# Kernel tuning notes

Hardware: AMD Instinct MI355X
Metric: run time of the kernel (lower is better)

## Reference

```python
import jax, jax.numpy as jnp
import numpy as np

D_MODEL = 2048
NUM_HEADS = 16
NUM_KV_HEADS = 4
HEAD_DIM = D_MODEL // NUM_HEADS          # 128
GROUPS = NUM_HEADS // NUM_KV_HEADS       # 4
ROT_DIM = HEAD_DIM // 2                  # 64
QK_EPS = 1e-6
B, L = 2, 2048


def setup_inputs() -> dict:
    key = jax.random.key(0)
    kx, kq, kk, kv, ko = jax.random.split(key, 5)
    x = jax.random.normal(kx, (B, L, D_MODEL), dtype=jnp.float32)
    # realistic RoPE tables, broadcastable against [B, L, H, ROT_DIM]
    inv_freq = 1.0 / (10000.0 ** (np.arange(ROT_DIM, dtype=np.float32) / ROT_DIM))
    ang = np.arange(L, dtype=np.float32)[:, None] * inv_freq[None, :]   # [L, ROT_DIM]
    cos = jnp.asarray(np.cos(ang), dtype=jnp.float32)[None, :, None, :]
    sin = jnp.asarray(np.sin(ang), dtype=jnp.float32)[None, :, None, :]
    s = 1.0 / np.sqrt(D_MODEL)
    Wq = jax.random.normal(kq, (D_MODEL, D_MODEL), dtype=jnp.float32) * s
    Wk = jax.random.normal(kk, (D_MODEL, NUM_KV_HEADS * HEAD_DIM), dtype=jnp.float32) * s
    Wv = jax.random.normal(kv, (D_MODEL, NUM_KV_HEADS * HEAD_DIM), dtype=jnp.float32) * s
    Wo = jax.random.normal(ko, (D_MODEL, D_MODEL), dtype=jnp.float32) * s
    return {"x": x, "cos": cos, "sin": sin, "Wq": Wq, "Wk": Wk, "Wv": Wv, "Wo": Wo}


def _apply_rope(t, cos, sin):
    # t: [B, L, H, HEAD_DIM]; half-split rotation as in the original
    x1, x2 = t[..., :ROT_DIM], t[..., ROT_DIM:]
    return jnp.concatenate([x1 * cos - x2 * sin, x2 * cos + x1 * sin], axis=-1)


def _rms_norm(t):
    ms = jnp.mean(jnp.square(t), axis=-1, keepdims=True)
    return t * jax.lax.rsqrt(ms + QK_EPS)


def reference(x, cos, sin, Wq, Wk, Wv, Wo):
    b, l, _ = x.shape
    q = (x @ Wq).reshape(b, l, NUM_HEADS, HEAD_DIM)
    k = (x @ Wk).reshape(b, l, NUM_KV_HEADS, HEAD_DIM)
    v = (x @ Wv).reshape(b, l, NUM_KV_HEADS, HEAD_DIM)
    q = _apply_rope(q, cos, sin)
    k = _apply_rope(k, cos, sin)
    # qk_norm=True: RMS-normalize q and k over head_dim
    q = _rms_norm(q)
    k = _rms_norm(k)
    # GQA: repeat kv heads to match q heads (matches reshape/tile/reshape)
    k = jnp.repeat(k, GROUPS, axis=2)   # [b, l, NUM_HEADS, HEAD_DIM]
    v = jnp.repeat(v, GROUPS, axis=2)
    scores = jnp.einsum('blhd,bmhd->bhlm', q, k) / np.float32(np.sqrt(HEAD_DIM))
    causal = jnp.tril(jnp.ones((l, l), dtype=bool))[None, None, :, :]
    scores = jnp.where(causal, scores, jnp.float32(-1e9))
    attn = jax.nn.softmax(scores, axis=-1)            # [b, h, l(q), m(kv)]
    out = jnp.einsum('bhlm,bmhd->blhd', attn, v).reshape(b, l, D_MODEL)
    return out @ Wo
```

## Files before the change

kernel.cpp:

```cpp
#include <hip/hip_runtime.h>
#include <stdint.h>

#define D_MODEL 2048
#define L_SEQ   2048
#define BATCH   2
#define NH      16
#define NKV     4
#define HD      128
#define ROT     64
#define M_ROWS  (BATCH * L_SEQ)
#define N_QKV   (D_MODEL + 2 * NKV * HD)

typedef short bf16x8 __attribute__((ext_vector_type(8)));
typedef float f32x4  __attribute__((ext_vector_type(4)));
typedef float f32x16 __attribute__((ext_vector_type(16)));

__device__ __forceinline__ unsigned short f2b(float f) {
  union { float f; unsigned u; } v; v.f = f;
  unsigned r = v.u + 0x7FFFu + ((v.u >> 16) & 1u);
  return (unsigned short)(r >> 16);
}

__device__ __forceinline__ unsigned cvtpk_bf16(float a, float b) {
  unsigned r;
  asm("v_cvt_pk_bf16_f32 %0, %1, %2" : "=v"(r) : "v"(a), "v"(b));
  return r;
}

__global__ void cvt_bf16_kernel(const float* __restrict__ in,
                                unsigned short* __restrict__ out, int n4) {
  int i = blockIdx.x * blockDim.x + threadIdx.x;
  if (i < n4) {
    float4 v = ((const float4*)in)[i];
    ushort4 o;
    o.x = f2b(v.x); o.y = f2b(v.y); o.z = f2b(v.z); o.w = f2b(v.w);
    ((ushort4*)out)[i] = o;
  }
}

__global__ void build_wqkv_t(const float* __restrict__ Wq, const float* __restrict__ Wk,
                             const float* __restrict__ Wv, unsigned short* __restrict__ Wt) {
  __shared__ float tile[32][33];
  int k0 = blockIdx.x * 32;
  int n0 = blockIdx.y * 32;
  const float* W; int c0, ldw;
  if (n0 < D_MODEL)            { W = Wq; c0 = n0;                 ldw = D_MODEL; }
  else if (n0 < D_MODEL + 512) { W = Wk; c0 = n0 - D_MODEL;       ldw = 512; }
  else                         { W = Wv; c0 = n0 - D_MODEL - 512; ldw = 512; }
  int tx = threadIdx.x, ty = threadIdx.y;
#pragma unroll
  for (int i = 0; i < 32; i += 8)
    tile[ty + i][tx] = W[(size_t)(k0 + ty + i) * ldw + c0 + tx];
  __syncthreads();
#pragma unroll
  for (int i = 0; i < 32; i += 8)
    Wt[(size_t)(n0 + ty + i) * D_MODEL + k0 + tx] = f2b(tile[tx][ty + i]);
}

__global__ void build_wo_t(const float* __restrict__ Wo, unsigned short* __restrict__ Wt) {
  __shared__ float tile[32][33];
  int k0 = blockIdx.x * 32;
  int n0 = blockIdx.y * 32;
  int tx = threadIdx.x, ty = threadIdx.y;
#pragma unroll
  for (int i = 0; i < 32; i += 8)
    tile[ty + i][tx] = Wo[(size_t)(k0 + ty + i) * D_MODEL + n0 + tx];
  __syncthreads();
#pragma unroll
  for (int i = 0; i < 32; i += 8)
    Wt[(size_t)(n0 + ty + i) * D_MODEL + k0 + tx] = f2b(tile[tx][ty + i]);
}

#define BM 128
#define BN 128
#define BKg 64

__device__ __forceinline__ void async16(void* lds, const void* g) {
  __builtin_amdgcn_global_load_lds((const __attribute__((address_space(1))) void*)g,
                                   (__attribute__((address_space(3))) void*)lds, 16, 0, 0);
}

__global__ __launch_bounds__(256, 2)
void gemm_bt(const unsigned short* __restrict__ A, const unsigned short* __restrict__ Bt,
             float* __restrict__ C, int M, int N, int K) {
  __shared__ unsigned short As[BM * BKg];
  __shared__ unsigned short Bs[BN * BKg];
  int m0 = blockIdx.y * BM;
  int n0 = blockIdx.x * BN;
  int tid = threadIdx.x;
  int lane = tid & 63;
  int wave = __builtin_amdgcn_readfirstlane(tid >> 6);
  int wr = wave >> 1, wc = wave & 1;
  int lgrp = lane >> 4, lidx = lane & 15;

  f32x4 acc[4][4];
#pragma unroll
  for (int i = 0; i < 4; i++)
#pragma unroll
    for (int j = 0; j < 4; j++) { acc[i][j][0]=0.f; acc[i][j][1]=0.f; acc[i][j][2]=0.f; acc[i][j][3]=0.f; }

  for (int k0 = 0; k0 < K; k0 += BKg) {
#pragma unroll
    for (int iss = 0; iss < 4; iss++) {
      int idx = iss * 256 + tid;
      int row = idx >> 3, cch = idx & 7;
      int lbase = (iss * 256 + wave * 64) * 8;
      async16((void*)(As + lbase), A  + (size_t)(m0 + row) * K + k0 + cch * 8);
      async16((void*)(Bs + lbase), Bt + (size_t)(n0 + row) * K + k0 + cch * 8);
    }
    __syncthreads();
#pragma unroll
    for (int kk = 0; kk < BKg; kk += 32) {
      bf16x8 af[4], bfr[4];
#pragma unroll
      for (int i = 0; i < 4; i++) {
        af[i]  = *(const bf16x8*)(As + (wr * 64 + i * 16 + lidx) * BKg + kk + lgrp * 8);
        bfr[i] = *(const bf16x8*)(Bs + (wc * 64 + i * 16 + lidx) * BKg + kk + lgrp * 8);
      }
#pragma unroll
      for (int i = 0; i < 4; i++)
#pragma unroll
        for (int j = 0; j < 4; j++)
          acc[i][j] = __builtin_amdgcn_mfma_f32_16x16x32_bf16(af[i], bfr[j], acc[i][j], 0, 0, 0);
    }
    __syncthreads();
  }
#pragma unroll
  for (int i = 0; i < 4; i++) {
    int rowb = m0 + wr * 64 + i * 16 + lgrp * 4;
#pragma unroll
    for (int j = 0; j < 4; j++) {
      int col = n0 + wc * 64 + j * 16 + lidx;
#pragma unroll
      for (int r = 0; r < 4; r++)
        C[(size_t)(rowb + r) * N + col] = acc[i][j][r];
    }
  }
}

__global__ __launch_bounds__(256)
void rope_rms_kernel(const float* __restrict__ QKV, const float* __restrict__ cosp,
                     const float* __restrict__ sinp, unsigned short* __restrict__ Qb,
                     unsigned short* __restrict__ Kb) {
  int row = blockIdx.x;
  int b = row >> 11, l = row & 2047;
  int lane = threadIdx.x & 63;
  int wave = threadIdx.x >> 6;
  const float* src = QKV + (size_t)row * N_QKV;
  float c = cosp[l * ROT + lane];
  float s = sinp[l * ROT + lane];
  for (int hh = wave; hh < NH + NKV; hh += 4) {
    bool isq = hh < NH;
    int col0 = isq ? hh * HD : D_MODEL + (hh - NH) * HD;
    float x1 = src[col0 + lane];
    float x2 = src[col0 + 64 + lane];
    float o1 = x1 * c - x2 * s;
    float o2 = x2 * c + x1 * s;
    float ss = o1 * o1 + o2 * o2;
#pragma unroll
    for (int mk = 1; mk < 64; mk <<= 1) ss += __shfl_xor(ss, mk, 64);
    float rn = rsqrtf(ss * (1.f / 128.f) + 1e-6f);
    if (isq) rn *= 0.08838834764831845f;
    o1 *= rn; o2 *= rn;
    unsigned short* dst = isq ? (Qb + ((size_t)(b * NH + hh) * L_SEQ + l) * HD)
                              : (Kb + ((size_t)(b * NKV + (hh - NH)) * L_SEQ + l) * HD);
    dst[lane]      = f2b(o1);
    dst[lane + 64] = f2b(o2);
  }
}

__global__ void vt_build(const float* __restrict__ QKV, unsigned short* __restrict__ Vt) {
  __shared__ float tile[32][33];
  int z = blockIdx.z;
  int l0 = blockIdx.x * 32;
  int d0 = blockIdx.y * 32;
  int b = z >> 2, kh = z & 3;
  int tx = threadIdx.x, ty = threadIdx.y;
  int colbase = D_MODEL + NKV * HD + kh * HD + d0;
#pragma unroll
  for (int i = 0; i < 32; i += 8)
    tile[ty + i][tx] = QKV[(size_t)(b * L_SEQ + l0 + ty + i) * N_QKV + colbase + tx];
  __syncthreads();
#pragma unroll
  for (int i = 0; i < 32; i += 8)
    Vt[((size_t)z * HD + d0 + ty + i) * L_SEQ + l0 + tx] = f2b(tile[tx][ty + i]);
}

__global__ __launch_bounds__(64)
void attn32_kernel(const unsigned short* __restrict__ Qb, const unsigned short* __restrict__ Kb,
                   const unsigned short* __restrict__ Vt, unsigned short* __restrict__ AttO) {
  __shared__ float tr[32][33];
  int idx = blockIdx.x;
  int qb = 63 - (idx >> 5);
  int bh = idx & 31;
  int b = bh >> 4, h = bh & 15, kh = h >> 2;
  int q0 = qb * 32;
  int lane = threadIdx.x;
  int col = lane & 31;
  int hi  = lane >> 5;

  const unsigned short* Q = Qb + ((size_t)(b * NH + h) * L_SEQ + q0) * HD;
  const unsigned short* K = Kb + (size_t)(b * NKV + kh) * L_SEQ * HD;
  const unsigned short* V = Vt + (size_t)(b * NKV + kh) * HD * L_SEQ;

  bf16x8 qf[8];
#pragma unroll
  for (int c = 0; c < 8; c++)
    qf[c] = *(const bf16x8*)(Q + (size_t)col * HD + c * 16 + hi * 8);

  f32x16 o[4];
#pragma unroll
  for (int d0 = 0; d0 < 4; d0++)
#pragma unroll
    for (int r = 0; r < 16; r++) o[d0][r] = 0.f;

  float m = -1e30f, lsum = 0.f;

  for (int kv0 = 0; kv0 <= q0; kv0 += 32) {
    f32x16 s;
#pragma unroll
    for (int r = 0; r < 16; r++) s[r] = 0.f;
#pragma unroll
    for (int c = 0; c < 8; c++) {
      bf16x8 kf = *(const bf16x8*)(K + (size_t)(kv0 + col) * HD + c * 16 + hi * 8);
      s = __builtin_amdgcn_mfma_f32_32x32x16_bf16(kf, qf[c], s, 0, 0, 0);
    }
    if (kv0 == q0) {
#pragma unroll
      for (int r = 0; r < 16; r++) {
        int kvl = (r & 3) + 8 * (r >> 2) + 4 * hi;
        if (kvl > col) s[r] = -1e30f;
      }
    }
    float mx = s[0];
#pragma unroll
    for (int r = 1; r < 16; r++) mx = fmaxf(mx, s[r]);
    mx = fmaxf(mx, __shfl_xor(mx, 32, 64));
    if (!__all(mx <= m + 8.f)) {
      float mnew = fmaxf(m, mx);
      float sf = __expf(m - mnew);
      lsum *= sf;
#pragma unroll
      for (int d0 = 0; d0 < 4; d0++)
#pragma unroll
        for (int r = 0; r < 16; r++) o[d0][r] *= sf;
      m = mnew;
    }
    float p[16];
    float ps = 0.f;
#pragma unroll
    for (int r = 0; r < 16; r++) { p[r] = __expf(s[r] - m); ps += p[r]; }
    lsum += ps + __shfl_xor(ps, 32, 64);
#pragma unroll
    for (int w = 0; w < 2; w++) {
      unsigned c01 = cvtpk_bf16(p[w*8+0], p[w*8+1]);
      unsigned c23 = cvtpk_bf16(p[w*8+2], p[w*8+3]);
      unsigned c45 = cvtpk_bf16(p[w*8+4], p[w*8+5]);
      unsigned c67 = cvtpk_bf16(p[w*8+6], p[w*8+7]);
      unsigned x01 = (unsigned)__shfl_xor((int)c01, 32, 64);
      unsigned x23 = (unsigned)__shfl_xor((int)c23, 32, 64);
      unsigned x45 = (unsigned)__shfl_xor((int)c45, 32, 64);
      unsigned x67 = (unsigned)__shfl_xor((int)c67, 32, 64);
      union { unsigned u[4]; bf16x8 v; } pb;
      pb.u[0] = hi ? x45 : c01;
      pb.u[1] = hi ? x67 : c23;
      pb.u[2] = hi ? c45 : x01;
      pb.u[3] = hi ? c67 : x23;
#pragma unroll
      for (int d0 = 0; d0 < 4; d0++) {
        bf16x8 vf = *(const bf16x8*)(V + (size_t)(d0 * 32 + col) * L_SEQ + kv0 + w * 16 + hi * 8);
        o[d0] = __builtin_amdgcn_mfma_f32_32x32x16_bf16(vf, pb.v, o[d0], 0, 0, 0);
      }
    }
  }

  float inv = 1.f / lsum;
  unsigned short* orow = AttO + (size_t)(b * L_SEQ + q0 + col) * D_MODEL + h * HD;
#pragma unroll
  for (int d0 = 0; d0 < 4; d0++) {
#pragma unroll
    for (int r = 0; r < 16; r++)
      tr[(r & 3) + 8 * (r >> 2) + 4 * hi][col] = o[d0][r] * inv;
    __syncthreads();
    union { unsigned u[8]; } pk;
#pragma unroll
    for (int t = 0; t < 8; t++) {
      float a  = tr[hi * 16 + 2 * t][col];
      float bb = tr[hi * 16 + 2 * t + 1][col];
      pk.u[t] = ((unsigned)f2b(a)) | (((unsigned)f2b(bb)) << 16);
    }
    *(uint4*)(orow + d0 * 32 + hi * 16)     = *(uint4*)&pk.u[0];
    *(uint4*)(orow + d0 * 32 + hi * 16 + 8) = *(uint4*)&pk.u[4];
    __syncthreads();
  }
}

extern "C" void kernel_launch(void* const* d_in, const int* in_sizes, int n_in,
                              void* d_out, int out_size, void* d_ws, size_t ws_size,
                              hipStream_t stream) {
  const float* x    = (const float*)d_in[0];
  const float* cosp = (const float*)d_in[1];
  const float* sinp = (const float*)d_in[2];
  const float* Wq   = (const float*)d_in[3];
  const float* Wk   = (const float*)d_in[4];
  const float* Wv   = (const float*)d_in[5];
  const float* Wo   = (const float*)d_in[6];
  float* out = (float*)d_out;

  char* ws = (char*)d_ws;
  unsigned short* Xb   = (unsigned short*)ws; ws += (size_t)M_ROWS * D_MODEL * 2;
  unsigned short* Wt   = (unsigned short*)ws; ws += (size_t)N_QKV * D_MODEL * 2;
  unsigned short* Wot  = (unsigned short*)ws; ws += (size_t)D_MODEL * D_MODEL * 2;
  float*          QKV  = (float*)ws;          ws += (size_t)M_ROWS * N_QKV * 4;
  unsigned short* Qb   = (unsigned short*)ws; ws += (size_t)BATCH * NH * L_SEQ * HD * 2;
  unsigned short* Kb   = (unsigned short*)ws; ws += (size_t)BATCH * NKV * L_SEQ * HD * 2;
  unsigned short* Vt   = (unsigned short*)ws; ws += (size_t)BATCH * NKV * HD * L_SEQ * 2;
  unsigned short* AttO = (unsigned short*)ws; ws += (size_t)M_ROWS * D_MODEL * 2;

  cvt_bf16_kernel<<<(M_ROWS * D_MODEL / 4 + 255) / 256, 256, 0, stream>>>(x, Xb, M_ROWS * D_MODEL / 4);
  build_wqkv_t<<<dim3(64, 96), dim3(32, 8), 0, stream>>>(Wq, Wk, Wv, Wt);
  build_wo_t<<<dim3(64, 64), dim3(32, 8), 0, stream>>>(Wo, Wot);
  gemm_bt<<<dim3(N_QKV / BN, M_ROWS / BM), 256, 0, stream>>>(Xb, Wt, QKV, M_ROWS, N_QKV, D_MODEL);
  rope_rms_kernel<<<M_ROWS, 256, 0, stream>>>(QKV, cosp, sinp, Qb, Kb);
  vt_build<<<dim3(64, 4, 8), dim3(32, 8), 0, stream>>>(QKV, Vt);
  attn32_kernel<<<dim3(64 * 32), 64, 0, stream>>>(Qb, Kb, Vt, AttO);
  gemm_bt<<<dim3(D_MODEL / BN, M_ROWS / BM), 256, 0, stream>>>(AttO, Wot, out, M_ROWS, D_MODEL, D_MODEL);
}
```

Baseline: 395.5 us.

## Share K/V tiles across four waves via double-buffered async LDS staging

Replaces the one-wave, 32-query attention kernel with a 256-thread block covering 128 query rows. Each K/V tile is loaded once into XOR-swizzled LDS by async copies and shared by four waves, double-buffered so the next tile loads while the current one is computed. The QK dot product is also split into two independent MFMA accumulator chains. This cuts redundant global/L2 traffic for K and V, but adds block-wide barriers each tile and leaves waves idle on the causal tail tiles. It relies on an async16 helper being defined elsewhere in the file.

```diff
diff --git a/kernel.cpp b/kernel.cpp
--- a/kernel.cpp
+++ b/kernel.cpp
@@ -186,22 +186,28 @@
     Vt[((size_t)z * HD + d0 + ty + i) * L_SEQ + l0 + tx] = f2b(tile[tx][ty + i]);
 }
 
-__global__ __launch_bounds__(64)
-void attn32_kernel(const unsigned short* __restrict__ Qb, const unsigned short* __restrict__ Kb,
-                   const unsigned short* __restrict__ Vt, unsigned short* __restrict__ AttO) {
-  __shared__ float tr[32][33];
-  int idx = blockIdx.x;
-  int qb = 63 - (idx >> 5);
-  int bh = idx & 31;
+#define KSTRIDE 256
+#define VSTRIDE 64
+#define TILEB   16384
+
+__global__ __launch_bounds__(256, 2)
+void attn128_kernel(const unsigned short* __restrict__ Qb, const unsigned short* __restrict__ Kb,
+                    const unsigned short* __restrict__ Vt, unsigned short* __restrict__ AttO) {
+  __shared__ char lds[2 * TILEB];
+  int blk = blockIdx.x;
+  int qt = 15 - (blk >> 5);
+  int bh = blk & 31;
   int b = bh >> 4, h = bh & 15, kh = h >> 2;
-  int q0 = qb * 32;
-  int lane = threadIdx.x;
+  int tid = threadIdx.x;
+  int lane = tid & 63;
+  int wave = __builtin_amdgcn_readfirstlane(tid >> 6);
   int col = lane & 31;
   int hi  = lane >> 5;
-
-  const unsigned short* Q = Qb + ((size_t)(b * NH + h) * L_SEQ + q0) * HD;
-  const unsigned short* K = Kb + (size_t)(b * NKV + kh) * L_SEQ * HD;
-  const unsigned short* V = Vt + (size_t)(b * NKV + kh) * HD * L_SEQ;
+  int q0 = qt * 128 + wave * 32;
+
+  const unsigned short* Q   = Qb + ((size_t)(b * NH + h) * L_SEQ + q0) * HD;
+  const unsigned short* Kg  = Kb + (size_t)(b * NKV + kh) * L_SEQ * HD;
+  const unsigned short* Vtg = Vt + (size_t)(b * NKV + kh) * HD * L_SEQ;
 
   bf16x8 qf[8];
 #pragma unroll
@@ -213,80 +219,122 @@
   for (int d0 = 0; d0 < 4; d0++)
 #pragma unroll
     for (int r = 0; r < 16; r++) o[d0][r] = 0.f;
-
   float m = -1e30f, lsum = 0.f;
 
-  for (int kv0 = 0; kv0 <= q0; kv0 += 32) {
-    f32x16 s;
-#pragma unroll
-    for (int r = 0; r < 16; r++) s[r] = 0.f;
-#pragma unroll
-    for (int c = 0; c < 8; c++) {
-      bf16x8 kf = *(const bf16x8*)(K + (size_t)(kv0 + col) * HD + c * 16 + hi * 8);
-      s = __builtin_amdgcn_mfma_f32_32x32x16_bf16(kf, qf[c], s, 0, 0, 0);
-    }
-    if (kv0 == q0) {
-#pragma unroll
-      for (int r = 0; r < 16; r++) {
-        int kvl = (r & 3) + 8 * (r >> 2) + 4 * hi;
-        if (kvl > col) s[r] = -1e30f;
-      }
-    }
-    float mx = s[0];
-#pragma unroll
-    for (int r = 1; r < 16; r++) mx = fmaxf(mx, s[r]);
-    mx = fmaxf(mx, __shfl_xor(mx, 32, 64));
-    if (!__all(mx <= m + 8.f)) {
-      float mnew = fmaxf(m, mx);
-      float sf = __expf(m - mnew);
-      lsum *= sf;
-#pragma unroll
-      for (int d0 = 0; d0 < 4; d0++)
-#pragma unroll
-        for (int r = 0; r < 16; r++) o[d0][r] *= sf;
-      m = mnew;
-    }
-    float p[16];
-    float ps = 0.f;
-#pragma unroll
-    for (int r = 0; r < 16; r++) { p[r] = __expf(s[r] - m); ps += p[r]; }
-    lsum += ps + __shfl_xor(ps, 32, 64);
-#pragma unroll
-    for (int w = 0; w < 2; w++) {
-      unsigned c01 = cvtpk_bf16(p[w*8+0], p[w*8+1]);
-      unsigned c23 = cvtpk_bf16(p[w*8+2], p[w*8+3]);
-      unsigned c45 = cvtpk_bf16(p[w*8+4], p[w*8+5]);
-      unsigned c67 = cvtpk_bf16(p[w*8+6], p[w*8+7]);
-      unsigned x01 = (unsigned)__shfl_xor((int)c01, 32, 64);
-      unsigned x23 = (unsigned)__shfl_xor((int)c23, 32, 64);
-      unsigned x45 = (unsigned)__shfl_xor((int)c45, 32, 64);
-      unsigned x67 = (unsigned)__shfl_xor((int)c67, 32, 64);
-      union { unsigned u[4]; bf16x8 v; } pb;
-      pb.u[0] = hi ? x45 : c01;
-      pb.u[1] = hi ? x67 : c23;
-      pb.u[2] = hi ? c45 : x01;
-      pb.u[3] = hi ? c67 : x23;
-#pragma unroll
-      for (int d0 = 0; d0 < 4; d0++) {
-        bf16x8 vf = *(const bf16x8*)(V + (size_t)(d0 * 32 + col) * L_SEQ + kv0 + w * 16 + hi * 8);
-        o[d0] = __builtin_amdgcn_mfma_f32_32x32x16_bf16(vf, pb.v, o[d0], 0, 0, 0);
-      }
-    }
-  }
-
+  int NT = 4 * (qt + 1);
+  int tmax = 4 * qt + wave;
+
+  auto STAGE = [&](char* base, int t) {
+    int kv0 = t * 32;
+    char* ldsK = base;
+    char* ldsV = base + 8192;
+    int wb = wave * 64;
+#pragma unroll
+    for (int r = 0; r < 2; r++) {
+      int slot = r * 256 + tid;
+      int row = slot >> 4, s16 = slot & 15;
+      const char* src = (const char*)Kg + (size_t)(kv0 + row) * KSTRIDE + ((s16 ^ (row & 7)) << 4);
+      async16(ldsK + (size_t)(r * 256 + wb) * 16, src);
+    }
+#pragma unroll
+    for (int r = 0; r < 2; r++) {
+      int slot = r * 256 + tid;
+      int row = slot >> 2, s4 = slot & 3;
+      const char* src = (const char*)Vtg + (size_t)row * (L_SEQ * 2) + (size_t)kv0 * 2 + ((s4 ^ (row & 3)) << 4);
+      async16(ldsV + (size_t)(r * 256 + wb) * 16, src);
+    }
+  };
+
+  STAGE(lds, 0);
+  __syncthreads();
+
+  int cur = 0;
+  for (int t = 0; t < NT; t++) {
+    if (t + 1 < NT) STAGE(lds + (cur ^ 1) * TILEB, t + 1);
+
+    if (t <= tmax) {
+      const char* KB = lds + cur * TILEB;
+      const char* VB = KB + 8192;
+      int kv0 = t * 32;
+      f32x16 sA, sB;
+#pragma unroll
+      for (int r = 0; r < 16; r++) { sA[r] = 0.f; sB[r] = 0.f; }
+#pragma unroll
+      for (int c = 0; c < 4; c++) {
+        bf16x8 kf = *(const bf16x8*)(KB + col * KSTRIDE + ((32 * c + 16 * hi) ^ ((col & 7) << 4)));
+        sA = __builtin_amdgcn_mfma_f32_32x32x16_bf16(kf, qf[c], sA, 0, 0, 0);
+      }
+#pragma unroll
+      for (int c = 4; c < 8; c++) {
+        bf16x8 kf = *(const bf16x8*)(KB + col * KSTRIDE + ((32 * c + 16 * hi) ^ ((col & 7) << 4)));
+        sB = __builtin_amdgcn_mfma_f32_32x32x16_bf16(kf, qf[c], sB, 0, 0, 0);
+      }
+      f32x16 s = sA + sB;
+      if (t == tmax) {
+#pragma unroll
+        for (int r = 0; r < 16; r++) {
+          int kvl = (r & 3) + 8 * (r >> 2) + 4 * hi;
+          if (kvl > col) s[r] = -1e30f;
+        }
+      }
+      float mx = s[0];
+#pragma unroll
+      for (int r = 1; r < 16; r++) mx = fmaxf(mx, s[r]);
+      mx = fmaxf(mx, __shfl_xor(mx, 32, 64));
+      if (!__all(mx <= m + 8.f)) {
+        float mnew = fmaxf(m, mx);
+        float sf = __expf(m - mnew);
+        lsum *= sf;
+#pragma unroll
+        for (int d0 = 0; d0 < 4; d0++)
+#pragma unroll
+          for (int r = 0; r < 16; r++) o[d0][r] *= sf;
+        m = mnew;
+      }
+      float ps = 0.f;
+#pragma unroll
+      for (int r = 0; r < 16; r++) { s[r] = __expf(s[r] - m); ps += s[r]; }
+      lsum += ps + __shfl_xor(ps, 32, 64);
+#pragma unroll
+      for (int w2 = 0; w2 < 2; w2++) {
+        unsigned c01 = cvtpk_bf16(s[w2*8+0], s[w2*8+1]);
+        unsigned c23 = cvtpk_bf16(s[w2*8+2], s[w2*8+3]);
+        unsigned c45 = cvtpk_bf16(s[w2*8+4], s[w2*8+5]);
+        unsigned c67 = cvtpk_bf16(s[w2*8+6], s[w2*8+7]);
+        unsigned x01 = (unsigned)__shfl_xor((int)c01, 32, 64);
+        unsigned x23 = (unsigned)__shfl_xor((int)c23, 32, 64);
+        unsigned x45 = (unsigned)__shfl_xor((int)c45, 32, 64);
+        unsigned x67 = (unsigned)__shfl_xor((int)c67, 32, 64);
+        union { unsigned u[4]; bf16x8 v; } pb;
+        pb.u[0] = hi ? x45 : c01;
+        pb.u[1] = hi ? x67 : c23;
+        pb.u[2] = hi ? c45 : x01;
+        pb.u[3] = hi ? c67 : x23;
+#pragma unroll
+        for (int d0 = 0; d0 < 4; d0++) {
+          bf16x8 vf = *(const bf16x8*)(VB + (d0 * 32 + col) * VSTRIDE + ((32 * w2 + 16 * hi) ^ ((col & 3) << 4)));
+          o[d0] = __builtin_amdgcn_mfma_f32_32x32x16_bf16(vf, pb.v, o[d0], 0, 0, 0);
+        }
+      }
+    }
+    __syncthreads();
+    cur ^= 1;
+  }
+
+  float* tr = (float*)(lds + wave * 4352);
   float inv = 1.f / lsum;
   unsigned short* orow = AttO + (size_t)(b * L_SEQ + q0 + col) * D_MODEL + h * HD;
 #pragma unroll
   for (int d0 = 0; d0 < 4; d0++) {
 #pragma unroll
     for (int r = 0; r < 16; r++)
-      tr[(r & 3) + 8 * (r >> 2) + 4 * hi][col] = o[d0][r] * inv;
+      tr[((r & 3) + 8 * (r >> 2) + 4 * hi) * 33 + col] = o[d0][r] * inv;
     __syncthreads();
     union { unsigned u[8]; } pk;
 #pragma unroll
     for (int t = 0; t < 8; t++) {
-      float a  = tr[hi * 16 + 2 * t][col];
-      float bb = tr[hi * 16 + 2 * t + 1][col];
+      float a  = tr[(hi * 16 + 2 * t) * 33 + col];
+      float bb = tr[(hi * 16 + 2 * t + 1) * 33 + col];
       pk.u[t] = ((unsigned)f2b(a)) | (((unsigned)f2b(bb)) << 16);
     }
     *(uint4*)(orow + d0 * 32 + hi * 16)     = *(uint4*)&pk.u[0];
@@ -323,6 +371,6 @@
   gemm_bt<<<dim3(N_QKV / BN, M_ROWS / BM), 256, 0, stream>>>(Xb, Wt, QKV, M_ROWS, N_QKV, D_MODEL);
   rope_rms_kernel<<<M_ROWS, 256, 0, stream>>>(QKV, cosp, sinp, Qb, Kb);
   vt_build<<<dim3(64, 4, 8), dim3(32, 8), 0, stream>>>(QKV, Vt);
-  attn32_kernel<<<dim3(64 * 32), 64, 0, stream>>>(Qb, Kb, Vt, AttO);
+  attn128_kernel<<<dim3(512), 256, 0, stream>>>(Qb, Kb, Vt, AttO);
   gemm_bt<<<dim3(D_MODEL / BN, M_ROWS / BM), 256, 0, stream>>>(AttO, Wot, out, M_ROWS, D_MODEL, D_MODEL);
 }
```

Measured after the change: 338.5 us. 1.17x faster.
